# Performance work log

Measured on AMD Instinct MI355X. Metric: run time of the kernel, lower is better.

Reference implementation:

```python
import jax, jax.numpy as jnp
import numpy as np


def conv1d(x, w, b, pad):
    # x: (B, Cin, T), w: (Cout, Cin, K), b: (Cout,)
    y = jax.lax.conv_general_dilated(x, w, window_strides=(1,), padding=[(pad, pad)],
                                     dimension_numbers=('NCH', 'OIH', 'NCH'))
    return y + b[None, :, None]


def setup_inputs() -> dict:
    key = jax.random.key(0)
    ks = jax.random.split(key, 16)
    B, Cmel, Ctxt, Catt, T1, T2 = 16, 80, 256, 80, 800, 200
    s = 0.05
    return {
        'queries': jax.random.normal(ks[0], (B, Cmel, T1), jnp.float32),
        'keys': jax.random.normal(ks[1], (B, Ctxt, T2), jnp.float32),
        'attn_prior': jax.random.uniform(ks[2], (B, T1, T2), jnp.float32),
        # key_proj: Conv1d(256->512,k=3,pad=1) -> ReLU -> Conv1d(512->80,k=1)
        'kw1': jax.random.normal(ks[3], (Ctxt * 2, Ctxt, 3), jnp.float32) * s,
        'kb1': jax.random.normal(ks[4], (Ctxt * 2,), jnp.float32) * s,
        'kw2': jax.random.normal(ks[5], (Catt, Ctxt * 2, 1), jnp.float32) * s,
        'kb2': jax.random.normal(ks[6], (Catt,), jnp.float32) * s,
        # query_proj (3xconv): 80->160 k3 -> ReLU -> 160->80 k1 -> ReLU -> 80->80 k1
        'qw1': jax.random.normal(ks[7], (Cmel * 2, Cmel, 3), jnp.float32) * s,
        'qb1': jax.random.normal(ks[8], (Cmel * 2,), jnp.float32) * s,
        'qw2': jax.random.normal(ks[9], (Cmel, Cmel * 2, 1), jnp.float32) * s,
        'qb2': jax.random.normal(ks[10], (Cmel,), jnp.float32) * s,
        'qw3': jax.random.normal(ks[11], (Catt, Cmel, 1), jnp.float32) * s,
        'qb3': jax.random.normal(ks[12], (Catt,), jnp.float32) * s,
    }


def reference(queries, keys, attn_prior, kw1, kb1, kw2, kb2, qw1, qb1, qw2, qb2, qw3, qb3):
    # key encoder
    k = jax.nn.relu(conv1d(keys, kw1, kb1, pad=1))
    k = conv1d(k, kw2, kb2, pad=0)                      # (B, Catt, T2)
    # query encoder ('3xconv')
    q = jax.nn.relu(conv1d(queries, qw1, qb1, pad=1))
    q = jax.nn.relu(conv1d(q, qw2, qb2, pad=0))
    q = conv1d(q, qw3, qb3, pad=0)                      # (B, Catt, T1)
    # L2 distance over channels: ||q||^2 + ||k||^2 - 2 q.k (same math as broadcast (q-k)^2 sum)
    q2 = jnp.sum(q * q, axis=1)                         # (B, T1)
    k2 = jnp.sum(k * k, axis=1)                         # (B, T2)
    qk = jnp.einsum('bct,bcs->bts', q, k)               # (B, T1, T2)
    attn = -0.0005 * (q2[:, :, None] + k2[:, None, :] - 2.0 * qk)[:, None]  # (B,1,T1,T2)
    attn = jax.nn.log_softmax(attn, axis=3) + jnp.log(attn_prior[:, None] + 1e-8)
    return attn
```

## Files before the change

kernel.cpp:

```cpp
#include <hip/hip_runtime.h>
#include <cstdint>
#include <cmath>

using short8  = __attribute__((ext_vector_type(8))) short;
using short4v = __attribute__((ext_vector_type(4))) short;
using floatx4 = __attribute__((ext_vector_type(4))) float;

__device__ __forceinline__ short f2bf(float f) {
  union { float f; unsigned u; } x; x.f = f;
  unsigned r = x.u + 0x7FFFu + ((x.u >> 16) & 1u);
  return (short)(r >> 16);
}

__global__ __launch_bounds__(256) void prep_kernel(
    const float* __restrict__ keys, const float* __restrict__ queries,
    const float* __restrict__ kw1, const float* __restrict__ kw2,
    const float* __restrict__ qw1, const float* __restrict__ qw2,
    const float* __restrict__ qw3,
    short* __restrict__ kT0, short* __restrict__ qT0,
    short* __restrict__ w1, short* __restrict__ w2, short* __restrict__ w3,
    short* __restrict__ w4, short* __restrict__ w5)
{
  const int bid = blockIdx.x, tid = threadIdx.x;
  __shared__ float xs[32][65];

  if (bid < 1136) {
    const float* src; short* dst; int CIN, T, CP, bx, by, b;
    if (bid < 512) {
      src = keys; dst = kT0; CIN = 256; T = 200; CP = 256;
      bx = bid & 3; by = (bid >> 2) & 7; b = bid >> 5;
    } else {
      int b2 = bid - 512;
      src = queries; dst = qT0; CIN = 80; T = 800; CP = 96;
      bx = b2 % 13; by = (b2 / 13) % 3; b = b2 / 39;
    }
    const int t0 = bx * 64, ci0 = by * 32;
    for (int i = tid; i < 32 * 64; i += 256) {
      int row = i >> 6, col = i & 63;
      float v = 0.f;
      if (ci0 + row < CIN && t0 + col < T)
        v = src[((size_t)b * CIN + ci0 + row) * T + t0 + col];
      xs[row][col] = v;
    }
    __syncthreads();
    int t = tid >> 2, c8 = (tid & 3) * 8;
    if (t0 + t < T) {
      short8 o;
      #pragma unroll
      for (int j = 0; j < 8; ++j) o[j] = f2bf(xs[c8 + j][t]);
      *(short8*)&dst[((size_t)b * T + t0 + t) * CP + ci0 + c8] = o;
    }
  } else {
    int blk = bid - 1136;
    const float* src; short* dst; int base;
    int CoP, CiP, Cout, CIN, K;
    if      (blk < 384) { src=kw1; dst=w1; base=0;   CoP=512; CiP=256; Cout=512; CIN=256; K=3; }
    else if (blk < 432) { src=kw2; dst=w2; base=384; CoP=96;  CiP=512; Cout=80;  CIN=512; K=1; }
    else if (blk < 486) { src=qw1; dst=w3; base=432; CoP=192; CiP=96;  Cout=160; CIN=80;  K=3; }
    else if (blk < 504) { src=qw2; dst=w4; base=486; CoP=96;  CiP=192; Cout=80;  CIN=160; K=1; }
    else                { src=qw3; dst=w5; base=504; CoP=96;  CiP=96;  Cout=80;  CIN=80;  K=1; }
    int tot = K * CoP * CiP;
    int b0 = (blk - base) * 1024;
    for (int e = 0; e < 4; ++e) {
      int gi = b0 + e * 256 + tid;
      if (gi < tot) {
        int dk  = gi / (CoP * CiP);
        int rem = gi - dk * (CoP * CiP);
        int co  = rem / CiP, ci = rem - (rem / CiP) * CiP;
        float v = (co < Cout && ci < CIN) ? src[((size_t)co * CIN + ci) * K + dk] : 0.f;
        dst[gi] = f2bf(v);
      }
    }
  }
}

__global__ __launch_bounds__(256) void conv_k3_kernel(
    const short* __restrict__ kT0, const short* __restrict__ qT0,
    const short* __restrict__ w1, const short* __restrict__ w3,
    const short* __restrict__ w4, const short* __restrict__ w5,
    const float* __restrict__ kb1, const float* __restrict__ qb1,
    const float* __restrict__ qb2, const float* __restrict__ qb3,
    short* __restrict__ kT1, short* __restrict__ qF)
{
  __shared__ __align__(16) short smem[18576];
  const int tid = threadIdx.x, wid = tid >> 6, lane = tid & 63;
  const int q = lane >> 4, m = lane & 15;

  if (blockIdx.x < 512) {
    const int blk = blockIdx.x;
    const int b = blk >> 5, co0 = ((blk >> 2) & 7) * 64, t0 = (blk & 3) * 64;
    const int wy = wid >> 1, wx = wid & 1;
    short* xs = smem;
    short* as = smem + 4752;

    floatx4 acc[2][2];
    #pragma unroll
    for (int i = 0; i < 2; ++i)
      #pragma unroll
      for (int j = 0; j < 2; ++j) acc[i][j] = (floatx4){0.f, 0.f, 0.f, 0.f};

    for (int c0 = 0; c0 < 4; ++c0) {
      __syncthreads();
      for (int i = tid; i < 66 * 8; i += 256) {
        int row = i >> 3, g = i & 7;
        int t = t0 + row - 1;
        int4 v = {0, 0, 0, 0};
        if (t >= 0 && t < 200)
          v = *(const int4*)&kT0[((size_t)b * 200 + t) * 256 + c0 * 64 + g * 8];
        *(int4*)&xs[row * 72 + g * 8] = v;
      }
      for (int i = tid; i < 192 * 8; i += 256) {
        int row = i >> 3, g = i & 7;
        int dk = row >> 6, co = row & 63;
        *(int4*)&as[row * 72 + g * 8] =
            *(const int4*)&w1[((size_t)(dk * 512 + co0 + co)) * 256 + c0 * 64 + g * 8];
      }
      __syncthreads();
      #pragma unroll
      for (int s = 0; s < 2; ++s) {
        #pragma unroll
        for (int dk = 0; dk < 3; ++dk) {
          short8 fa0 = *(const short8*)&as[(dk * 64 + wy * 32 + m) * 72 + s * 32 + q * 8];
          short8 fa1 = *(const short8*)&as[(dk * 64 + wy * 32 + 16 + m) * 72 + s * 32 + q * 8];
          #pragma unroll
          for (int j = 0; j < 2; ++j) {
            short8 fb = *(const short8*)&xs[(wx * 32 + j * 16 + m + dk) * 72 + s * 32 + q * 8];
            acc[0][j] = __builtin_amdgcn_mfma_f32_16x16x32_bf16(fa0, fb, acc[0][j], 0, 0, 0);
            acc[1][j] = __builtin_amdgcn_mfma_f32_16x16x32_bf16(fa1, fb, acc[1][j], 0, 0, 0);
          }
        }
      }
    }
    #pragma unroll
    for (int i = 0; i < 2; ++i) {
      #pragma unroll
      for (int j = 0; j < 2; ++j) {
        #pragma unroll
        for (int r = 0; r < 4; ++r) {
          int co = co0 + wy * 32 + i * 16 + q * 4 + r;
          int t  = t0 + wx * 32 + j * 16 + m;
          if (t < 200) {
            float v = fmaxf(acc[i][j][r] + kb1[co], 0.f);
            kT1[((size_t)b * 200 + t) * 512 + co] = f2bf(v);
          }
        }
      }
    }
  } else {
    const int qbid = blockIdx.x - 512;
    const int b = qbid / 13, t0 = (qbid % 13) * 64;
    short* xs  = smem;
    short* y1c = smem + 2640;
    short* y2c = y1c;

    floatx4 accq[3][4];
    #pragma unroll
    for (int f = 0; f < 3; ++f)
      #pragma unroll
      for (int tf = 0; tf < 4; ++tf) accq[f][tf] = (floatx4){0.f, 0.f, 0.f, 0.f};

    for (int c0 = 0; c0 < 3; ++c0) {
      __syncthreads();
      for (int i = tid; i < 66 * 4; i += 256) {
        int row = i >> 2, c8 = (i & 3) * 8;
        int t = t0 + row - 1;
        int4 v = {0, 0, 0, 0};
        if (t >= 0 && t < 800)
          v = *(const int4*)&qT0[((size_t)b * 800 + t) * 96 + c0 * 32 + c8];
        *(int4*)&xs[row * 40 + c8] = v;
      }
      __syncthreads();
      #pragma unroll
      for (int dk = 0; dk < 3; ++dk) {
        short8 fa[3];
        #pragma unroll
        for (int f = 0; f < 3; ++f)
          fa[f] = *(const short8*)&w3[((size_t)(dk * 192 + wid * 48 + f * 16 + m)) * 96
                                      + c0 * 32 + q * 8];
        #pragma unroll
        for (int tf = 0; tf < 4; ++tf) {
          short8 fb = *(const short8*)&xs[(tf * 16 + m + dk) * 40 + q * 8];
          #pragma unroll
          for (int f = 0; f < 3; ++f)
            accq[f][tf] = __builtin_amdgcn_mfma_f32_16x16x32_bf16(fa[f], fb, accq[f][tf], 0, 0, 0);
        }
      }
    }
    __syncthreads();
    #pragma unroll
    for (int f = 0; f < 3; ++f) {
      #pragma unroll
      for (int tf = 0; tf < 4; ++tf) {
        int co = wid * 48 + f * 16 + q * 4;
        int t  = tf * 16 + m;
        short4v o;
        #pragma unroll
        for (int r = 0; r < 4; ++r) {
          float bv = (co + r < 160) ? qb1[co + r] : 0.f;
          o[r] = f2bf(fmaxf(accq[f][tf][r] + bv, 0.f));
        }
        *(short4v*)&y1c[(co >> 5) * 2560 + t * 40 + (co & 31)] = o;
      }
    }
    __syncthreads();

    floatx4 acc2q[6];
    #pragma unroll
    for (int f = 0; f < 6; ++f) acc2q[f] = (floatx4){0.f, 0.f, 0.f, 0.f};
    #pragma unroll
    for (int c = 0; c < 6; ++c) {
      short8 fb = *(const short8*)&y1c[c * 2560 + (wid * 16 + m) * 40 + q * 8];
      #pragma unroll
      for (int f = 0; f < 6; ++f) {
        short8 fa = *(const short8*)&w4[((size_t)(f * 16 + m)) * 192 + c * 32 + q * 8];
        acc2q[f] = __builtin_amdgcn_mfma_f32_16x16x32_bf16(fa, fb, acc2q[f], 0, 0, 0);
      }
    }
    __syncthreads();
    #pragma unroll
    for (int f = 0; f < 6; ++f) {
      int co = f * 16 + q * 4;
      int t  = wid * 16 + m;
      short4v o;
      #pragma unroll
      for (int r = 0; r < 4; ++r) {
        float bv = (co + r < 80) ? qb2[co + r] : 0.f;
        o[r] = f2bf(fmaxf(acc2q[f][r] + bv, 0.f));
      }
      *(short4v*)&y2c[(co >> 5) * 2560 + t * 40 + (co & 31)] = o;
    }
    __syncthreads();

    floatx4 acc3q[6];
    #pragma unroll
    for (int f = 0; f < 6; ++f) acc3q[f] = (floatx4){0.f, 0.f, 0.f, 0.f};
    #pragma unroll
    for (int c = 0; c < 3; ++c) {
      short8 fb = *(const short8*)&y2c[c * 2560 + (wid * 16 + m) * 40 + q * 8];
      #pragma unroll
      for (int f = 0; f < 6; ++f) {
        short8 fa = *(const short8*)&w5[((size_t)(f * 16 + m)) * 96 + c * 32 + q * 8];
        acc3q[f] = __builtin_amdgcn_mfma_f32_16x16x32_bf16(fa, fb, acc3q[f], 0, 0, 0);
      }
    }
    int t = t0 + wid * 16 + m;
    if (t < 800) {
      #pragma unroll
      for (int f = 0; f < 6; ++f) {
        int co = f * 16 + q * 4;
        short4v o;
        #pragma unroll
        for (int r = 0; r < 4; ++r) {
          float bv = (co + r < 80) ? qb3[co + r] : 0.f;
          o[r] = f2bf(acc3q[f][r] + bv);
        }
        *(short4v*)&qF[((size_t)b * 800 + t) * 96 + co] = o;
      }
    }
  }
}

__global__ __launch_bounds__(256) void kconv2_kernel(
    const short* __restrict__ kT1, const short* __restrict__ w2,
    const float* __restrict__ kb2, short* __restrict__ kF)
{
  const int blk = blockIdx.x;
  const int b = blk >> 2, t0 = (blk & 3) * 64;
  const int tid = threadIdx.x, wid = tid >> 6, lane = tid & 63;
  const int q = lane >> 4, m = lane & 15;
  const int t = t0 + wid * 16 + m;
  const bool tv = (t < 200);

  floatx4 acc[6];
  #pragma unroll
  for (int f = 0; f < 6; ++f) acc[f] = (floatx4){0.f, 0.f, 0.f, 0.f};

  #pragma unroll
  for (int c = 0; c < 16; ++c) {
    short8 fb;
    if (tv) fb = *(const short8*)&kT1[((size_t)b * 200 + t) * 512 + c * 32 + q * 8];
    else    fb = (short8){0,0,0,0,0,0,0,0};
    #pragma unroll
    for (int f = 0; f < 6; ++f) {
      short8 fa = *(const short8*)&w2[((size_t)(f * 16 + m)) * 512 + c * 32 + q * 8];
      acc[f] = __builtin_amdgcn_mfma_f32_16x16x32_bf16(fa, fb, acc[f], 0, 0, 0);
    }
  }
  if (tv) {
    #pragma unroll
    for (int f = 0; f < 6; ++f) {
      int co = f * 16 + q * 4;
      short4v o;
      #pragma unroll
      for (int r = 0; r < 4; ++r) {
        float bv = (co + r < 80) ? kb2[co + r] : 0.f;
        o[r] = f2bf(acc[f][r] + bv);
      }
      *(short4v*)&kF[((size_t)b * 200 + t) * 96 + co] = o;
    }
  }
}

__global__ __launch_bounds__(256) void attn_mfma(
    const short* __restrict__ qT, const short* __restrict__ kT,
    const float* __restrict__ prior, float* __restrict__ out)
{
  const int b = blockIdx.y, t1_0 = blockIdx.x * 64;
  const int tid = threadIdx.x, wid = tid >> 6, lane = tid & 63;
  const int q = lane >> 4, m = lane & 15;

  __shared__ __align__(16) short aq[64 * 104];
  __shared__ __align__(16) short bk[208 * 104];
  __shared__ float k2s[208];

  for (int i = tid; i < 64 * 12; i += 256) {
    int row = i / 12, g = i - (i / 12) * 12;
    int4 v = {0, 0, 0, 0};
    if (t1_0 + row < 800)
      v = *(const int4*)&qT[((size_t)b * 800 + t1_0 + row) * 96 + g * 8];
    *(int4*)&aq[row * 104 + g * 8] = v;
  }
  for (int i = tid; i < 208 * 12; i += 256) {
    int row = i / 12, g = i - (i / 12) * 12;
    int4 v = {0, 0, 0, 0};
    if (row < 200)
      v = *(const int4*)&kT[((size_t)b * 200 + row) * 96 + g * 8];
    *(int4*)&bk[row * 104 + g * 8] = v;
  }
  __syncthreads();

  if (tid < 208) {
    float k2acc = 0.f;
    #pragma unroll
    for (int g = 0; g < 12; ++g) {
      short8 s = *(const short8*)&bk[tid * 104 + g * 8];
      #pragma unroll
      for (int j = 0; j < 8; ++j) {
        union { unsigned u; float f; } x; x.u = ((unsigned)(unsigned short)s[j]) << 16;
        k2acc = fmaf(x.f, x.f, k2acc);
      }
    }
    k2s[tid] = k2acc;
  }

  floatx4 acc[13];
  #pragma unroll
  for (int f = 0; f < 13; ++f) acc[f] = (floatx4){0.f, 0.f, 0.f, 0.f};

  #pragma unroll
  for (int c = 0; c < 3; ++c) {
    short8 fa = *(const short8*)&aq[(wid * 16 + m) * 104 + c * 32 + q * 8];
    #pragma unroll
    for (int f = 0; f < 13; ++f) {
      short8 fb = *(const short8*)&bk[(f * 16 + m) * 104 + c * 32 + q * 8];
      acc[f] = __builtin_amdgcn_mfma_f32_16x16x32_bf16(fa, fb, acc[f], 0, 0, 0);
    }
  }
  __syncthreads();

  float k2v[13];
  #pragma unroll
  for (int f = 0; f < 13; ++f) k2v[f] = k2s[f * 16 + m];

  float mx[4] = {-INFINITY, -INFINITY, -INFINITY, -INFINITY};
  #pragma unroll
  for (int f = 0; f < 13; ++f) {
    bool valid = (f * 16 + m) < 200;
    #pragma unroll
    for (int r = 0; r < 4; ++r) {
      float v = valid ? (0.001f * acc[f][r] - 0.0005f * k2v[f]) : -INFINITY;
      acc[f][r] = v;
      mx[r] = fmaxf(mx[r], v);
    }
  }
  #pragma unroll
  for (int msk = 1; msk < 16; msk <<= 1)
    #pragma unroll
    for (int r = 0; r < 4; ++r) mx[r] = fmaxf(mx[r], __shfl_xor(mx[r], msk));
  float sm[4] = {0.f, 0.f, 0.f, 0.f};
  #pragma unroll
  for (int f = 0; f < 13; ++f)
    #pragma unroll
    for (int r = 0; r < 4; ++r) sm[r] += __expf(acc[f][r] - mx[r]);
  #pragma unroll
  for (int msk = 1; msk < 16; msk <<= 1)
    #pragma unroll
    for (int r = 0; r < 4; ++r) sm[r] += __shfl_xor(sm[r], msk);
  float lse[4];
  #pragma unroll
  for (int r = 0; r < 4; ++r) lse[r] = mx[r] + __logf(sm[r]);

  #pragma unroll
  for (int f = 0; f < 13; ++f) {
    int col = f * 16 + m;
    if (col < 200) {
      #pragma unroll
      for (int r = 0; r < 4; ++r) {
        int t1 = t1_0 + wid * 16 + q * 4 + r;
        if (t1 < 800) {
          size_t o = ((size_t)b * 800 + t1) * 200 + col;
          out[o] = acc[f][r] - lse[r] + __logf(prior[o] + 1e-8f);
        }
      }
    }
  }
}

extern "C" void kernel_launch(void* const* d_in, const int* in_sizes, int n_in,
                              void* d_out, int out_size, void* d_ws, size_t ws_size,
                              hipStream_t stream) {
  const float* queries = (const float*)d_in[0];
  const float* keys    = (const float*)d_in[1];
  const float* prior   = (const float*)d_in[2];
  const float* kw1 = (const float*)d_in[3];
  const float* kb1 = (const float*)d_in[4];
  const float* kw2 = (const float*)d_in[5];
  const float* kb2 = (const float*)d_in[6];
  const float* qw1 = (const float*)d_in[7];
  const float* qb1 = (const float*)d_in[8];
  const float* qw2 = (const float*)d_in[9];
  const float* qb2 = (const float*)d_in[10];
  const float* qw3 = (const float*)d_in[11];
  const float* qb3 = (const float*)d_in[12];
  float* out = (float*)d_out;

  short* p = (short*)d_ws;
  short* kT0 = p;  p += (size_t)3200 * 256;
  short* qT0 = p;  p += (size_t)12800 * 96;
  short* w1  = p;  p += (size_t)3 * 512 * 256;
  short* w2  = p;  p += (size_t)96 * 512;
  short* w3  = p;  p += (size_t)3 * 192 * 96;
  short* w4  = p;  p += (size_t)96 * 192;
  short* w5  = p;  p += (size_t)96 * 96;
  short* kT1 = p;  p += (size_t)3200 * 512;
  short* kF  = p;  p += (size_t)3200 * 96;
  short* qF  = p;  p += (size_t)12800 * 96;

  prep_kernel<<<dim3(1649), 256, 0, stream>>>(keys, queries, kw1, kw2, qw1, qw2, qw3,
                                              kT0, qT0, w1, w2, w3, w4, w5);
  conv_k3_kernel<<<dim3(720), 256, 0, stream>>>(kT0, qT0, w1, w3, w4, w5,
                                                kb1, qb1, qb2, qb3, kT1, qF);
  kconv2_kernel<<<dim3(64), 256, 0, stream>>>(kT1, w2, kb2, kF);
  attn_mfma<<<dim3(13, 16), 256, 0, stream>>>(qF, kF, prior, out);
}
```

Measured before the change: 156.0 us.

## Shrink key conv tiles and split kconv2 channel reduction across waves

The key k=3 conv tile shrinks from 64x64 to 64 output channels by 32 timesteps, one 16-row slice per wave, raising the grid from 512 to 896 key blocks. kconv2 moves from 64 blocks to 208 by giving each wave a quarter of the input channels and reducing the partial sums through shared memory. Both changes aim to fill more compute units on small, underutilised stages. In exchange, weight reloads per output rise, and kconv2 gains an LDS reduction and a barrier.

New measurement: 158.9 us. Within noise of the previous version (+1.9%).

```diff
diff --git a/kernel.cpp b/kernel.cpp
--- a/kernel.cpp
+++ b/kernel.cpp
@@ -74,7 +74,7 @@
   }
 }
 
-__global__ __launch_bounds__(256) void conv_k3_kernel(
+__global__ __launch_bounds__(256) void encoders_kernel(
     const short* __restrict__ kT0, const short* __restrict__ qT0,
     const short* __restrict__ w1, const short* __restrict__ w3,
     const short* __restrict__ w4, const short* __restrict__ w5,
@@ -83,25 +83,23 @@
     short* __restrict__ kT1, short* __restrict__ qF)
 {
   __shared__ __align__(16) short smem[18576];
-  const int tid = threadIdx.x, wid = tid >> 6, lane = tid & 63;
+  const int tid = threadIdx.x, wv = tid >> 6, lane = tid & 63;
   const int q = lane >> 4, m = lane & 15;
 
-  if (blockIdx.x < 512) {
+  if (blockIdx.x < 896) {
     const int blk = blockIdx.x;
-    const int b = blk >> 5, co0 = ((blk >> 2) & 7) * 64, t0 = (blk & 3) * 64;
-    const int wy = wid >> 1, wx = wid & 1;
+    const int b = blk / 56, rem = blk % 56;
+    const int co0 = (rem / 7) * 64, t0 = (rem % 7) * 32;
     short* xs = smem;
-    short* as = smem + 4752;
-
-    floatx4 acc[2][2];
-    #pragma unroll
-    for (int i = 0; i < 2; ++i)
-      #pragma unroll
-      for (int j = 0; j < 2; ++j) acc[i][j] = (floatx4){0.f, 0.f, 0.f, 0.f};
+    short* as = smem + 2448;
+
+    floatx4 acc[2];
+    acc[0] = (floatx4){0.f, 0.f, 0.f, 0.f};
+    acc[1] = (floatx4){0.f, 0.f, 0.f, 0.f};
 
     for (int c0 = 0; c0 < 4; ++c0) {
       __syncthreads();
-      for (int i = tid; i < 66 * 8; i += 256) {
+      for (int i = tid; i < 34 * 8; i += 256) {
         int row = i >> 3, g = i & 7;
         int t = t0 + row - 1;
         int4 v = {0, 0, 0, 0};
@@ -117,37 +115,32 @@
       }
       __syncthreads();
       #pragma unroll
-      for (int s = 0; s < 2; ++s) {
-        #pragma unroll
-        for (int dk = 0; dk < 3; ++dk) {
-          short8 fa0 = *(const short8*)&as[(dk * 64 + wy * 32 + m) * 72 + s * 32 + q * 8];
-          short8 fa1 = *(const short8*)&as[(dk * 64 + wy * 32 + 16 + m) * 72 + s * 32 + q * 8];
+      for (int dk = 0; dk < 3; ++dk) {
+        #pragma unroll
+        for (int ks = 0; ks < 2; ++ks) {
+          short8 fa = *(const short8*)&as[(dk * 64 + wv * 16 + m) * 72 + ks * 32 + q * 8];
           #pragma unroll
           for (int j = 0; j < 2; ++j) {
-            short8 fb = *(const short8*)&xs[(wx * 32 + j * 16 + m + dk) * 72 + s * 32 + q * 8];
-            acc[0][j] = __builtin_amdgcn_mfma_f32_16x16x32_bf16(fa0, fb, acc[0][j], 0, 0, 0);
-            acc[1][j] = __builtin_amdgcn_mfma_f32_16x16x32_bf16(fa1, fb, acc[1][j], 0, 0, 0);
+            short8 fb = *(const short8*)&xs[(j * 16 + m + dk) * 72 + ks * 32 + q * 8];
+            acc[j] = __builtin_amdgcn_mfma_f32_16x16x32_bf16(fa, fb, acc[j], 0, 0, 0);
           }
         }
       }
     }
-    #pragma unroll
-    for (int i = 0; i < 2; ++i) {
-      #pragma unroll
-      for (int j = 0; j < 2; ++j) {
-        #pragma unroll
-        for (int r = 0; r < 4; ++r) {
-          int co = co0 + wy * 32 + i * 16 + q * 4 + r;
-          int t  = t0 + wx * 32 + j * 16 + m;
-          if (t < 200) {
-            float v = fmaxf(acc[i][j][r] + kb1[co], 0.f);
-            kT1[((size_t)b * 200 + t) * 512 + co] = f2bf(v);
-          }
-        }
+    const int co = co0 + wv * 16 + q * 4;
+    const floatx4 bv = *(const floatx4*)&kb1[co];
+    #pragma unroll
+    for (int j = 0; j < 2; ++j) {
+      int t = t0 + j * 16 + m;
+      if (t < 200) {
+        short4v o;
+        #pragma unroll
+        for (int r = 0; r < 4; ++r) o[r] = f2bf(fmaxf(acc[j][r] + bv[r], 0.f));
+        *(short4v*)&kT1[((size_t)b * 200 + t) * 512 + co] = o;
       }
     }
   } else {
-    const int qbid = blockIdx.x - 512;
+    const int qbid = blockIdx.x - 896;
     const int b = qbid / 13, t0 = (qbid % 13) * 64;
     short* xs  = smem;
     short* y1c = smem + 2640;
@@ -175,7 +168,7 @@
         short8 fa[3];
         #pragma unroll
         for (int f = 0; f < 3; ++f)
-          fa[f] = *(const short8*)&w3[((size_t)(dk * 192 + wid * 48 + f * 16 + m)) * 96
+          fa[f] = *(const short8*)&w3[((size_t)(dk * 192 + wv * 48 + f * 16 + m)) * 96
                                       + c0 * 32 + q * 8];
         #pragma unroll
         for (int tf = 0; tf < 4; ++tf) {
@@ -191,7 +184,7 @@
     for (int f = 0; f < 3; ++f) {
       #pragma unroll
       for (int tf = 0; tf < 4; ++tf) {
-        int co = wid * 48 + f * 16 + q * 4;
+        int co = wv * 48 + f * 16 + q * 4;
         int t  = tf * 16 + m;
         short4v o;
         #pragma unroll
@@ -209,7 +202,7 @@
     for (int f = 0; f < 6; ++f) acc2q[f] = (floatx4){0.f, 0.f, 0.f, 0.f};
     #pragma unroll
     for (int c = 0; c < 6; ++c) {
-      short8 fb = *(const short8*)&y1c[c * 2560 + (wid * 16 + m) * 40 + q * 8];
+      short8 fb = *(const short8*)&y1c[c * 2560 + (wv * 16 + m) * 40 + q * 8];
       #pragma unroll
       for (int f = 0; f < 6; ++f) {
         short8 fa = *(const short8*)&w4[((size_t)(f * 16 + m)) * 192 + c * 32 + q * 8];
@@ -220,7 +213,7 @@
     #pragma unroll
     for (int f = 0; f < 6; ++f) {
       int co = f * 16 + q * 4;
-      int t  = wid * 16 + m;
+      int t  = wv * 16 + m;
       short4v o;
       #pragma unroll
       for (int r = 0; r < 4; ++r) {
@@ -236,14 +229,14 @@
     for (int f = 0; f < 6; ++f) acc3q[f] = (floatx4){0.f, 0.f, 0.f, 0.f};
     #pragma unroll
     for (int c = 0; c < 3; ++c) {
-      short8 fb = *(const short8*)&y2c[c * 2560 + (wid * 16 + m) * 40 + q * 8];
+      short8 fb = *(const short8*)&y2c[c * 2560 + (wv * 16 + m) * 40 + q * 8];
       #pragma unroll
       for (int f = 0; f < 6; ++f) {
         short8 fa = *(const short8*)&w5[((size_t)(f * 16 + m)) * 96 + c * 32 + q * 8];
         acc3q[f] = __builtin_amdgcn_mfma_f32_16x16x32_bf16(fa, fb, acc3q[f], 0, 0, 0);
       }
     }
-    int t = t0 + wid * 16 + m;
+    int t = t0 + wv * 16 + m;
     if (t < 800) {
       #pragma unroll
       for (int f = 0; f < 6; ++f) {
@@ -264,11 +257,11 @@
     const short* __restrict__ kT1, const short* __restrict__ w2,
     const float* __restrict__ kb2, short* __restrict__ kF)
 {
-  const int blk = blockIdx.x;
-  const int b = blk >> 2, t0 = (blk & 3) * 64;
-  const int tid = threadIdx.x, wid = tid >> 6, lane = tid & 63;
+  __shared__ float kacc[4][96 * 16];
+  const int b = blockIdx.y, t0 = blockIdx.x * 16;
+  const int tid = threadIdx.x, wv = tid >> 6, lane = tid & 63;
   const int q = lane >> 4, m = lane & 15;
-  const int t = t0 + wid * 16 + m;
+  const int t = t0 + m;
   const bool tv = (t < 200);
 
   floatx4 acc[6];
@@ -276,7 +269,8 @@
   for (int f = 0; f < 6; ++f) acc[f] = (floatx4){0.f, 0.f, 0.f, 0.f};
 
   #pragma unroll
-  for (int c = 0; c < 16; ++c) {
+  for (int e = 0; e < 4; ++e) {
+    int c = wv * 4 + e;
     short8 fb;
     if (tv) fb = *(const short8*)&kT1[((size_t)b * 200 + t) * 512 + c * 32 + q * 8];
     else    fb = (short8){0,0,0,0,0,0,0,0};
@@ -286,17 +280,20 @@
       acc[f] = __builtin_amdgcn_mfma_f32_16x16x32_bf16(fa, fb, acc[f], 0, 0, 0);
     }
   }
-  if (tv) {
-    #pragma unroll
-    for (int f = 0; f < 6; ++f) {
-      int co = f * 16 + q * 4;
-      short4v o;
-      #pragma unroll
-      for (int r = 0; r < 4; ++r) {
-        float bv = (co + r < 80) ? kb2[co + r] : 0.f;
-        o[r] = f2bf(acc[f][r] + bv);
-      }
-      *(short4v*)&kF[((size_t)b * 200 + t) * 96 + co] = o;
+  #pragma unroll
+  for (int f = 0; f < 6; ++f)
+    #pragma unroll
+    for (int r = 0; r < 4; ++r)
+      kacc[wv][(f * 16 + q * 4 + r) * 16 + m] = acc[f][r];
+  __syncthreads();
+
+  for (int i = tid; i < 1536; i += 256) {
+    int tt = i / 96, co = i - (i / 96) * 96;
+    if (t0 + tt < 200) {
+      float s = kacc[0][co * 16 + tt] + kacc[1][co * 16 + tt]
+              + kacc[2][co * 16 + tt] + kacc[3][co * 16 + tt];
+      if (co < 80) s += kb2[co];
+      kF[((size_t)b * 200 + t0 + tt) * 96 + co] = f2bf(s);
     }
   }
 }
@@ -425,21 +422,21 @@
   float* out = (float*)d_out;
 
   short* p = (short*)d_ws;
-  short* kT0 = p;  p += (size_t)3200 * 256;
-  short* qT0 = p;  p += (size_t)12800 * 96;
   short* w1  = p;  p += (size_t)3 * 512 * 256;
   short* w2  = p;  p += (size_t)96 * 512;
   short* w3  = p;  p += (size_t)3 * 192 * 96;
   short* w4  = p;  p += (size_t)96 * 192;
   short* w5  = p;  p += (size_t)96 * 96;
+  short* kT0 = p;  p += (size_t)3200 * 256;
+  short* qT0 = p;  p += (size_t)12800 * 96;
   short* kT1 = p;  p += (size_t)3200 * 512;
   short* kF  = p;  p += (size_t)3200 * 96;
   short* qF  = p;  p += (size_t)12800 * 96;
 
   prep_kernel<<<dim3(1649), 256, 0, stream>>>(keys, queries, kw1, kw2, qw1, qw2, qw3,
                                               kT0, qT0, w1, w2, w3, w4, w5);
-  conv_k3_kernel<<<dim3(720), 256, 0, stream>>>(kT0, qT0, w1, w3, w4, w5,
-                                                kb1, qb1, qb2, qb3, kT1, qF);
-  kconv2_kernel<<<dim3(64), 256, 0, stream>>>(kT1, w2, kb2, kF);
+  encoders_kernel<<<dim3(1104), 256, 0, stream>>>(kT0, qT0, w1, w3, w4, w5,
+                                                  kb1, qb1, qb2, qb3, kT1, qF);
+  kconv2_kernel<<<dim3(13, 16), 256, 0, stream>>>(kT1, w2, kb2, kF);
   attn_mfma<<<dim3(13, 16), 256, 0, stream>>>(qF, kF, prior, out);
 }
```
